# Kernel optimization log

Hardware: AMD Instinct MI355X
Metric: run time of the kernel (lower is better)

Reference implementation:

```python
import jax, jax.numpy as jnp
import numpy as np

N_GRAPHS = 64


def gcn_conv(x, W, b, src, dst, n_nodes):
    """PyG GCNConv: add self-loops, symmetric D^-1/2 (A+I) D^-1/2 normalization,
    linear transform, scatter-add aggregation at target nodes, plus bias."""
    xw = x @ W  # [N, out]  transform before propagate (PyG order)
    loop = jnp.arange(n_nodes, dtype=src.dtype)
    rows = jnp.concatenate([src, loop])  # message sources
    cols = jnp.concatenate([dst, loop])  # message targets
    deg = jax.ops.segment_sum(jnp.ones_like(cols, dtype=xw.dtype), cols,
                              num_segments=n_nodes)
    dinv = jnp.where(deg > 0, jax.lax.rsqrt(deg), 0.0)
    norm = dinv[rows] * dinv[cols]  # [E+N]
    msgs = norm[:, None] * xw[rows]  # gather + scale
    out = jax.ops.segment_sum(msgs, cols, num_segments=n_nodes)  # scatter-add
    return out + b


def global_mean_pool(x, batch, n_graphs):
    sums = jax.ops.segment_sum(x, batch, num_segments=n_graphs)
    cnts = jax.ops.segment_sum(jnp.ones((x.shape[0],), x.dtype), batch,
                               num_segments=n_graphs)
    return sums / jnp.maximum(cnts, 1.0)[:, None]


def setup_inputs() -> dict:
    key = jax.random.key(0)
    k1, k2, k3, k4, k5, k6 = jax.random.split(key, 6)
    N, E = 50000, 800000
    d_in, d_hid, d_out = 128, 128, 64
    x = jax.random.normal(k1, (N, d_in), dtype=jnp.float32)
    edge_index = jax.random.randint(k2, (2, E), 0, N, dtype=jnp.int64)
    batch = jnp.sort(jax.random.randint(k3, (N,), 0, N_GRAPHS, dtype=jnp.int64))
    # Glorot-ish init for GCN weights, zero bias (PyG default)
    W1 = jax.random.normal(k4, (d_in, d_hid), dtype=jnp.float32) / np.sqrt(d_in)
    b1 = jnp.zeros((d_hid,), jnp.float32)
    W2 = jax.random.normal(k5, (d_hid, d_out), dtype=jnp.float32) / np.sqrt(d_hid)
    b2 = jnp.zeros((d_out,), jnp.float32)
    return {"x": x, "edge_index": edge_index, "batch": batch,
            "W1": W1, "b1": b1, "W2": W2, "b2": b2}


def reference(x, edge_index, batch, W1, b1, W2, b2):
    n_nodes = x.shape[0]
    src, dst = edge_index[0], edge_index[1]
    h = jax.nn.relu(gcn_conv(x, W1, b1, src, dst, n_nodes))
    h = gcn_conv(h, W2, b2, src, dst, n_nodes)
    return global_mean_pool(h, batch, N_GRAPHS)
```

## Files before the change

### kernel.cpp

```cpp
#include <hip/hip_runtime.h>

typedef __attribute__((ext_vector_type(8))) short bf16x8;
typedef __attribute__((ext_vector_type(4))) float f32x4;

__device__ __forceinline__ unsigned short f2bf(float f) {
  unsigned u = __float_as_uint(f);
  u += 0x7FFFu + ((u >> 16) & 1u);
  return (unsigned short)(u >> 16);
}
__device__ __forceinline__ float bflo(unsigned u) { return __uint_as_float(u << 16); }
__device__ __forceinline__ float bfhi(unsigned u) { return __uint_as_float(u & 0xFFFF0000u); }

template <int CO, bool AF32>
__device__ __forceinline__ void gemm_body(const void* __restrict__ Aptr,
                                          const float* __restrict__ W,
                                          unsigned short* __restrict__ Y, int N,
                                          int bid, int tid, unsigned short* Wl) {
  constexpr int K = 128;
  constexpr int SP = K + 8;
  for (int i = tid; i < K * CO; i += 256) {
    int k = i / CO, n = i % CO;
    Wl[n * SP + k] = f2bf(W[i]);
  }
  __syncthreads();

  const int lane = tid & 63;
  const int quad = lane >> 4, l16 = lane & 15;
  const int mbase = bid * 64 + (tid >> 6) * 16;
  const int arow = min(mbase + l16, N - 1);

  bf16x8 afrag[4];
  if constexpr (AF32) {
    const float* A = (const float*)Aptr + (size_t)arow * K;
#pragma unroll
    for (int ks = 0; ks < 4; ks++) {
      const float4* p = (const float4*)(A + ks * 32 + quad * 8);
      float4 f0 = p[0], f1 = p[1];
      afrag[ks] = (bf16x8){(short)f2bf(f0.x), (short)f2bf(f0.y), (short)f2bf(f0.z), (short)f2bf(f0.w),
                           (short)f2bf(f1.x), (short)f2bf(f1.y), (short)f2bf(f1.z), (short)f2bf(f1.w)};
    }
  } else {
    const unsigned short* A = (const unsigned short*)Aptr + (size_t)arow * K;
#pragma unroll
    for (int ks = 0; ks < 4; ks++) afrag[ks] = *(const bf16x8*)(A + ks * 32 + quad * 8);
  }

#pragma unroll
  for (int ct = 0; ct < CO / 16; ct++) {
    f32x4 acc = {0.0f, 0.0f, 0.0f, 0.0f};
#pragma unroll
    for (int ks = 0; ks < 4; ks++) {
      bf16x8 b = *(const bf16x8*)(&Wl[(ct * 16 + l16) * SP + ks * 32 + quad * 8]);
      acc = __builtin_amdgcn_mfma_f32_16x16x32_bf16(afrag[ks], b, acc, 0, 0, 0);
    }
#pragma unroll
    for (int reg = 0; reg < 4; reg++) {
      int node = mbase + quad * 4 + reg;
      if (node < N) Y[(size_t)node * CO + ct * 16 + l16] = f2bf(acc[reg]);
    }
  }
}

__global__ __launch_bounds__(256) void k_mega1(const float* __restrict__ x,
                                               const float* __restrict__ W1,
                                               unsigned short* __restrict__ xw1b, int N,
                                               const int* __restrict__ dst,
                                               int* __restrict__ cnt,
                                               int* __restrict__ rank, int E,
                                               const int* __restrict__ batch,
                                               int* __restrict__ firstIdx,
                                               int gM, int gE4) {
  __shared__ unsigned short Wl[128 * 136];
  const int bid = blockIdx.x, tid = threadIdx.x;
  if (bid < gM) {
    gemm_body<128, true>(x, W1, xw1b, N, bid, tid, Wl);
  } else if (bid < gM + gE4) {
    int e0 = (bid - gM) * 1024 + tid * 4;
    if (e0 + 3 < E) {
      int4 d4 = *(const int4*)(dst + e0);
      int4 r;
      r.x = atomicAdd(&cnt[d4.x], 1);
      r.y = atomicAdd(&cnt[d4.y], 1);
      r.z = atomicAdd(&cnt[d4.z], 1);
      r.w = atomicAdd(&cnt[d4.w], 1);
      *(int4*)(rank + e0) = r;
    } else {
      for (int e = e0; e < E; e++) rank[e] = atomicAdd(&cnt[dst[e]], 1);
    }
  } else {
    int n = (bid - gM - gE4) * 256 + tid;
    if (n < N) {
      int b = batch[n];
      if (n == 0 || batch[n - 1] != b) firstIdx[b] = n + 1;
    }
  }
}

__global__ void k_seg(const int* __restrict__ cnt, int* __restrict__ start,
                      float* __restrict__ dinv, int* __restrict__ counter, int N) {
  const int v = blockIdx.x * 256 + threadIdx.x;
  const int lane = threadIdx.x & 63;
  int c = (v < N) ? cnt[v] : 0;
  int incl = c;
#pragma unroll
  for (int d = 1; d < 64; d <<= 1) {
    int t = __shfl_up(incl, d, 64);
    if (lane >= d) incl += t;
  }
  int base = 0;
  if (lane == 63) base = atomicAdd(counter, incl);
  base = __shfl(base, 63, 64);
  if (v < N) {
    start[v] = base + incl - c;
    dinv[v] = rsqrtf((float)(c + 1));
  }
}

__global__ void k_fill(const int* __restrict__ src, const int* __restrict__ dst,
                       const int* __restrict__ rank, const int* __restrict__ start,
                       const float* __restrict__ dinv, int2* __restrict__ colw, int E) {
  int e = blockIdx.x * 256 + threadIdx.x;
  if (e < E) {
    int s = src[e], d = dst[e];
    int p = start[d] + rank[e];
    float w = dinv[s] * dinv[d];
    colw[p] = make_int2(s, __float_as_int(w));
  }
}

__global__ __launch_bounds__(256) void k_agg128(const unsigned short* __restrict__ xwb,
                                                const float* __restrict__ dinv,
                                                const int* __restrict__ start,
                                                const int* __restrict__ cnt,
                                                const int2* __restrict__ colw,
                                                const float* __restrict__ bias,
                                                unsigned short* __restrict__ out, int N) {
  __shared__ int2 sEdge[4][64];
  const int tid = threadIdx.x;
  const int lane = tid & 63;
  const int wv = tid >> 6;
  const int slot = lane >> 4;
  const int fl = lane & 15;
  const int v = blockIdx.x * 4 + wv;
  if (v >= N) return;

  float acc[8] = {0.f, 0.f, 0.f, 0.f, 0.f, 0.f, 0.f, 0.f};
  const float dv = dinv[v];
  const float d2 = dv * dv;
  if (slot == 0) {
    uint4 s = *(const uint4*)((const char*)xwb + (((size_t)v << 8) | (fl << 4)));
    acc[0] += d2 * bflo(s.x); acc[1] += d2 * bfhi(s.x);
    acc[2] += d2 * bflo(s.y); acc[3] += d2 * bfhi(s.y);
    acc[4] += d2 * bflo(s.z); acc[5] += d2 * bfhi(s.z);
    acc[6] += d2 * bflo(s.w); acc[7] += d2 * bfhi(s.w);
  }

  const int j0 = start[v], jc = cnt[v];
  for (int base = 0; base < jc; base += 64) {
    int2 cw = (base + lane < jc) ? colw[j0 + base + lane] : make_int2(0, 0);
    sEdge[wv][lane] = cw;
    int m = jc - base;
    if (m > 64) m = 64;
    const int rounds = (m + 3) >> 2;
    const int rp = (rounds + 3) & ~3;
    for (int t = 0; t < rp; t += 4) {
      uint4 rbuf[4];
      float wbuf[4];
#pragma unroll
      for (int r = 0; r < 4; r++) {
        int2 e = sEdge[wv][(t + r) * 4 + slot];
        wbuf[r] = __int_as_float(e.y);
        rbuf[r] = *(const uint4*)((const char*)xwb + (((unsigned)e.x << 8) | (fl << 4)));
      }
#pragma unroll
      for (int r = 0; r < 4; r++) {
        const float w = wbuf[r];
        const uint4 rr = rbuf[r];
        acc[0] += w * bflo(rr.x); acc[1] += w * bfhi(rr.x);
        acc[2] += w * bflo(rr.y); acc[3] += w * bfhi(rr.y);
        acc[4] += w * bflo(rr.z); acc[5] += w * bfhi(rr.z);
        acc[6] += w * bflo(rr.w); acc[7] += w * bfhi(rr.w);
      }
    }
  }

#pragma unroll
  for (int d = 16; d < 64; d <<= 1)
#pragma unroll
    for (int k = 0; k < 8; k++) acc[k] += __shfl_xor(acc[k], d, 64);

  if (slot == 0) {
    float4 b0 = ((const float4*)bias)[fl * 2];
    float4 b1 = ((const float4*)bias)[fl * 2 + 1];
    float a0 = fmaxf(acc[0] + b0.x, 0.f), a1 = fmaxf(acc[1] + b0.y, 0.f);
    float a2 = fmaxf(acc[2] + b0.z, 0.f), a3 = fmaxf(acc[3] + b0.w, 0.f);
    float a4 = fmaxf(acc[4] + b1.x, 0.f), a5 = fmaxf(acc[5] + b1.y, 0.f);
    float a6 = fmaxf(acc[6] + b1.z, 0.f), a7 = fmaxf(acc[7] + b1.w, 0.f);
    uint4 st;
    st.x = (unsigned)f2bf(a0) | ((unsigned)f2bf(a1) << 16);
    st.y = (unsigned)f2bf(a2) | ((unsigned)f2bf(a3) << 16);
    st.z = (unsigned)f2bf(a4) | ((unsigned)f2bf(a5) << 16);
    st.w = (unsigned)f2bf(a6) | ((unsigned)f2bf(a7) << 16);
    *(uint4*)((char*)out + (((size_t)v << 8) | (fl << 4))) = st;
  }
}

__global__ __launch_bounds__(256) void k_gemm2(const unsigned short* __restrict__ A,
                                               const float* __restrict__ W,
                                               unsigned short* __restrict__ Y, int N) {
  __shared__ unsigned short Wl[64 * 136];
  gemm_body<64, false>(A, W, Y, N, blockIdx.x, threadIdx.x, Wl);
}

__global__ __launch_bounds__(256) void k_aggpool(const unsigned short* __restrict__ xwb,
                                                 const float* __restrict__ dinv,
                                                 const int* __restrict__ start,
                                                 const int* __restrict__ cnt,
                                                 const int2* __restrict__ colw,
                                                 const int* __restrict__ batch,
                                                 float* __restrict__ stage, int N) {
  __shared__ int2 sEdge[4][64];
  __shared__ float sAcc[4][64];
  const int tid = threadIdx.x;
  const int lane = tid & 63;
  const int wv = tid >> 6;
  const int slot = lane >> 3;
  const int fl = lane & 7;
  const int v = blockIdx.x * 4 + wv;

  float acc[8] = {0.f, 0.f, 0.f, 0.f, 0.f, 0.f, 0.f, 0.f};
  int b = 0;
  if (v < N) {
    b = batch[v];
    const float dv = dinv[v];
    const float d2 = dv * dv;
    if (slot == 0) {
      uint4 s = *(const uint4*)((const char*)xwb + (((size_t)v << 7) | (fl << 4)));
      acc[0] += d2 * bflo(s.x); acc[1] += d2 * bfhi(s.x);
      acc[2] += d2 * bflo(s.y); acc[3] += d2 * bfhi(s.y);
      acc[4] += d2 * bflo(s.z); acc[5] += d2 * bfhi(s.z);
      acc[6] += d2 * bflo(s.w); acc[7] += d2 * bfhi(s.w);
    }
    const int j0 = start[v], jc = cnt[v];
    for (int base = 0; base < jc; base += 64) {
      int2 cw = (base + lane < jc) ? colw[j0 + base + lane] : make_int2(0, 0);
      sEdge[wv][lane] = cw;
      int m = jc - base;
      if (m > 64) m = 64;
      const int rounds = (m + 7) >> 3;
      const int rp = (rounds + 3) & ~3;
      for (int t = 0; t < rp; t += 4) {
        uint4 rbuf[4];
        float wbuf[4];
#pragma unroll
        for (int r = 0; r < 4; r++) {
          int2 e = sEdge[wv][(t + r) * 8 + slot];
          wbuf[r] = __int_as_float(e.y);
          rbuf[r] = *(const uint4*)((const char*)xwb + (((unsigned)e.x << 7) | (fl << 4)));
        }
#pragma unroll
        for (int r = 0; r < 4; r++) {
          const float w = wbuf[r];
          const uint4 rr = rbuf[r];
          acc[0] += w * bflo(rr.x); acc[1] += w * bfhi(rr.x);
          acc[2] += w * bflo(rr.y); acc[3] += w * bfhi(rr.y);
          acc[4] += w * bflo(rr.z); acc[5] += w * bfhi(rr.z);
          acc[6] += w * bflo(rr.w); acc[7] += w * bfhi(rr.w);
        }
      }
    }
#pragma unroll
    for (int d = 8; d < 64; d <<= 1)
#pragma unroll
      for (int k = 0; k < 8; k++) acc[k] += __shfl_xor(acc[k], d, 64);
  }

  if (slot == 0) {
    *(float4*)&sAcc[wv][fl * 8] = make_float4(acc[0], acc[1], acc[2], acc[3]);
    *(float4*)&sAcc[wv][fl * 8 + 4] = make_float4(acc[4], acc[5], acc[6], acc[7]);
  }
  __syncthreads();

  const int v0 = blockIdx.x * 4;
  const int b0 = batch[min(v0, N - 1)];
  const int b3 = batch[min(v0 + 3, N - 1)];
  if ((b0 == b3) && (v0 + 3 < N)) {
    if (wv == 0) {
      float t = sAcc[0][lane] + sAcc[1][lane] + sAcc[2][lane] + sAcc[3][lane];
      atomicAdd(&stage[b0 * 64 + lane], t);
    }
  } else if (v < N) {
    atomicAdd(&stage[b * 64 + lane], sAcc[wv][lane]);
  }
}

__global__ void k_final(const float* __restrict__ stage, const int* __restrict__ firstIdx,
                        const float* __restrict__ b2, float* __restrict__ out, int N) {
  __shared__ float denom[64];
  const int tid = threadIdx.x;
  if (tid < 64) {
    int raw = firstIdx[tid];
    int fi = (raw > 0) ? raw - 1 : 0x7FFFFFFF;
    int m = fi;
#pragma unroll
    for (int d = 1; d < 64; d <<= 1) {
      int t = __shfl_down(m, d, 64);
      if (tid + d < 64) m = min(m, t);
    }
    int nxtm = __shfl_down(m, 1, 64);
    int nxt = (tid == 63) ? N : min(nxtm, N);
    int c = (fi == 0x7FFFFFFF) ? 0 : (nxt - fi);
    denom[tid] = fmaxf((float)c, 1.0f);
  }
  __syncthreads();
  for (int i = tid; i < 64 * 64; i += 256)
    out[i] = stage[i] / denom[i >> 6] + b2[i & 63];
}


extern "C" void kernel_launch(void* const* d_in, const int* in_sizes, int n_in,
                              void* d_out, int out_size, void* d_ws, size_t ws_size,
                              hipStream_t stream) {
  const float* x     = (const float*)d_in[0];
  const int*   ei    = (const int*)d_in[1];
  const int*   batch = (const int*)d_in[2];
  const float* W1    = (const float*)d_in[3];
  const float* b1    = (const float*)d_in[4];
  const float* W2    = (const float*)d_in[5];
  const float* b2    = (const float*)d_in[6];

  const int N = in_sizes[2];
  const int E = in_sizes[1] / 2;
  const int* src  = ei;
  const int* dstv = ei + E;

  unsigned short* xw1b = (unsigned short*)d_ws;
  unsigned short* h1b  = xw1b + (size_t)N * 128;
  unsigned short* xw2b = xw1b;
  int*   cnt     = (int*)(h1b + (size_t)N * 128);
  int*   counter = cnt + N;
  int*   firstIdx= counter + 1;
  float* stage   = (float*)(firstIdx + 64);
  int*   startv  = (int*)(stage + 4096);
  float* dinv    = (float*)(startv + N);
  int2*  colw    = (int2*)(((uintptr_t)(dinv + N) + 15) & ~(uintptr_t)15);
  int*   rank    = (int*)(colw + E);
  float* outp    = (float*)d_out;

  hipMemsetAsync(cnt, 0, (size_t)(N + 1 + 64 + 4096) * sizeof(int), stream);

  const int gM  = (N + 63) / 64;
  const int gE4 = (E + 1023) / 1024;
  const int gE  = (E + 255) / 256;
  const int gN  = (N + 255) / 256;
  const int gA  = (N + 3) / 4;

  k_mega1<<<gM + gE4 + gN, 256, 0, stream>>>(x, W1, xw1b, N, dstv, cnt, rank, E,
                                             batch, firstIdx, gM, gE4);
  k_seg<<<gN, 256, 0, stream>>>(cnt, startv, dinv, counter, N);
  k_fill<<<gE, 256, 0, stream>>>(src, dstv, rank, startv, dinv, colw, E);

  k_agg128<<<gA, 256, 0, stream>>>(xw1b, dinv, startv, cnt, colw, b1, h1b, N);

  k_gemm2<<<gM, 256, 0, stream>>>(h1b, W2, xw2b, N);
  k_aggpool<<<gA, 256, 0, stream>>>(xw2b, dinv, startv, cnt, colw, batch, stage, N);

  k_final<<<1, 256, 0, stream>>>(stage, firstIdx, b2, outp, N);
}
```

Before: 233.0 us.

## Map one node per lane-group in aggregation kernels, broadcast edges via shuffles

Both aggregation kernels now assign one destination node to each 16-lane (or 8-lane) group instead of one node per wavefront, so a wave processes 4 or 8 nodes at once. Edge metadata is loaded per group and broadcast with shuffles instead of being staged in shared memory, and the cross-group reduction is gone. This targets the lane waste that comes from low-degree nodes (about 16 edges on average) being spread across a full wave. The cost is divergence, since each wave iterates up to the largest degree in its group, and non-uniform pool blocks now issue per-element atomics.

```diff
diff --git a/kernel.cpp b/kernel.cpp
--- a/kernel.cpp
+++ b/kernel.cpp
@@ -135,42 +135,44 @@
                                                 const int2* __restrict__ colw,
                                                 const float* __restrict__ bias,
                                                 unsigned short* __restrict__ out, int N) {
-  __shared__ int2 sEdge[4][64];
   const int tid = threadIdx.x;
   const int lane = tid & 63;
+  const int gl = lane & 15;
+  const int grp = lane >> 4;
   const int wv = tid >> 6;
-  const int slot = lane >> 4;
-  const int fl = lane & 15;
-  const int v = blockIdx.x * 4 + wv;
-  if (v >= N) return;
-
-  float acc[8] = {0.f, 0.f, 0.f, 0.f, 0.f, 0.f, 0.f, 0.f};
-  const float dv = dinv[v];
-  const float d2 = dv * dv;
-  if (slot == 0) {
-    uint4 s = *(const uint4*)((const char*)xwb + (((size_t)v << 8) | (fl << 4)));
-    acc[0] += d2 * bflo(s.x); acc[1] += d2 * bfhi(s.x);
-    acc[2] += d2 * bflo(s.y); acc[3] += d2 * bfhi(s.y);
-    acc[4] += d2 * bflo(s.z); acc[5] += d2 * bfhi(s.z);
-    acc[6] += d2 * bflo(s.w); acc[7] += d2 * bfhi(s.w);
-  }
-
-  const int j0 = start[v], jc = cnt[v];
-  for (int base = 0; base < jc; base += 64) {
-    int2 cw = (base + lane < jc) ? colw[j0 + base + lane] : make_int2(0, 0);
-    sEdge[wv][lane] = cw;
-    int m = jc - base;
-    if (m > 64) m = 64;
-    const int rounds = (m + 3) >> 2;
-    const int rp = (rounds + 3) & ~3;
+  const int v = blockIdx.x * 16 + wv * 4 + grp;
+  const int vc = min(v, N - 1);
+
+  const float dv = dinv[vc];
+  const int j0 = start[vc];
+  const int jc = (v < N) ? cnt[vc] : 0;
+
+  float acc[8];
+  {
+    const float d2 = dv * dv;
+    uint4 s = *(const uint4*)((const char*)xwb + (((size_t)vc << 8) | (gl << 4)));
+    acc[0] = d2 * bflo(s.x); acc[1] = d2 * bfhi(s.x);
+    acc[2] = d2 * bflo(s.y); acc[3] = d2 * bfhi(s.y);
+    acc[4] = d2 * bflo(s.z); acc[5] = d2 * bfhi(s.z);
+    acc[6] = d2 * bflo(s.w); acc[7] = d2 * bfhi(s.w);
+  }
+
+  const int gbase = grp << 4;
+  for (int base = 0; __any(base < jc); base += 16) {
+    int2 cw = (base + gl < jc) ? colw[j0 + base + gl] : make_int2(0, 0);
+    int mv = jc - base;
+    mv = mv < 0 ? 0 : (mv > 16 ? 16 : mv);
+    int mm = max(mv, __shfl_xor(mv, 16, 64));
+    mm = max(mm, __shfl_xor(mm, 32, 64));
+    const int rp = (mm + 3) & ~3;
     for (int t = 0; t < rp; t += 4) {
       uint4 rbuf[4];
       float wbuf[4];
 #pragma unroll
       for (int r = 0; r < 4; r++) {
-        int2 e = sEdge[wv][(t + r) * 4 + slot];
-        wbuf[r] = __int_as_float(e.y);
-        rbuf[r] = *(const uint4*)((const char*)xwb + (((unsigned)e.x << 8) | (fl << 4)));
+        int sx = __shfl(cw.x, gbase + t + r, 64);
+        wbuf[r] = __int_as_float(__shfl(cw.y, gbase + t + r, 64));
+        rbuf[r] = *(const uint4*)((const char*)xwb + (((unsigned)sx << 8) | (gl << 4)));
       }
 #pragma unroll
       for (int r = 0; r < 4; r++) {
@@ -184,14 +186,9 @@
     }
   }
 
-#pragma unroll
-  for (int d = 16; d < 64; d <<= 1)
-#pragma unroll
-    for (int k = 0; k < 8; k++) acc[k] += __shfl_xor(acc[k], d, 64);
-
-  if (slot == 0) {
-    float4 b0 = ((const float4*)bias)[fl * 2];
-    float4 b1 = ((const float4*)bias)[fl * 2 + 1];
+  if (v < N) {
+    float4 b0 = ((const float4*)bias)[gl * 2];
+    float4 b1 = ((const float4*)bias)[gl * 2 + 1];
     float a0 = fmaxf(acc[0] + b0.x, 0.f), a1 = fmaxf(acc[1] + b0.y, 0.f);
     float a2 = fmaxf(acc[2] + b0.z, 0.f), a3 = fmaxf(acc[3] + b0.w, 0.f);
     float a4 = fmaxf(acc[4] + b1.x, 0.f), a5 = fmaxf(acc[5] + b1.y, 0.f);
@@ -201,7 +198,7 @@
     st.y = (unsigned)f2bf(a2) | ((unsigned)f2bf(a3) << 16);
     st.z = (unsigned)f2bf(a4) | ((unsigned)f2bf(a5) << 16);
     st.w = (unsigned)f2bf(a6) | ((unsigned)f2bf(a7) << 16);
-    *(uint4*)((char*)out + (((size_t)v << 8) | (fl << 4))) = st;
+    *(uint4*)((char*)out + (((size_t)v << 8) | (gl << 4))) = st;
   }
 }
 
@@ -219,78 +216,79 @@
                                                  const int2* __restrict__ colw,
                                                  const int* __restrict__ batch,
                                                  float* __restrict__ stage, int N) {
-  __shared__ int2 sEdge[4][64];
   __shared__ float sAcc[4][64];
   const int tid = threadIdx.x;
   const int lane = tid & 63;
+  const int gl = lane & 7;
+  const int grp = lane >> 3;
   const int wv = tid >> 6;
-  const int slot = lane >> 3;
-  const int fl = lane & 7;
-  const int v = blockIdx.x * 4 + wv;
-
-  float acc[8] = {0.f, 0.f, 0.f, 0.f, 0.f, 0.f, 0.f, 0.f};
-  int b = 0;
-  if (v < N) {
-    b = batch[v];
-    const float dv = dinv[v];
-    const float d2 = dv * dv;
-    if (slot == 0) {
-      uint4 s = *(const uint4*)((const char*)xwb + (((size_t)v << 7) | (fl << 4)));
-      acc[0] += d2 * bflo(s.x); acc[1] += d2 * bfhi(s.x);
-      acc[2] += d2 * bflo(s.y); acc[3] += d2 * bfhi(s.y);
-      acc[4] += d2 * bflo(s.z); acc[5] += d2 * bfhi(s.z);
-      acc[6] += d2 * bflo(s.w); acc[7] += d2 * bfhi(s.w);
-    }
-    const int j0 = start[v], jc = cnt[v];
-    for (int base = 0; base < jc; base += 64) {
-      int2 cw = (base + lane < jc) ? colw[j0 + base + lane] : make_int2(0, 0);
-      sEdge[wv][lane] = cw;
-      int m = jc - base;
-      if (m > 64) m = 64;
-      const int rounds = (m + 7) >> 3;
-      const int rp = (rounds + 3) & ~3;
-      for (int t = 0; t < rp; t += 4) {
-        uint4 rbuf[4];
-        float wbuf[4];
-#pragma unroll
-        for (int r = 0; r < 4; r++) {
-          int2 e = sEdge[wv][(t + r) * 8 + slot];
-          wbuf[r] = __int_as_float(e.y);
-          rbuf[r] = *(const uint4*)((const char*)xwb + (((unsigned)e.x << 7) | (fl << 4)));
-        }
-#pragma unroll
-        for (int r = 0; r < 4; r++) {
-          const float w = wbuf[r];
-          const uint4 rr = rbuf[r];
-          acc[0] += w * bflo(rr.x); acc[1] += w * bfhi(rr.x);
-          acc[2] += w * bflo(rr.y); acc[3] += w * bfhi(rr.y);
-          acc[4] += w * bflo(rr.z); acc[5] += w * bfhi(rr.z);
-          acc[6] += w * bflo(rr.w); acc[7] += w * bfhi(rr.w);
-        }
+  const int v = blockIdx.x * 32 + wv * 8 + grp;
+  const int vc = min(v, N - 1);
+
+  const float dv = dinv[vc];
+  const int j0 = start[vc];
+  const int jc = (v < N) ? cnt[vc] : 0;
+  const int b = batch[vc];
+
+  float acc[8];
+  {
+    const float d2 = (v < N) ? dv * dv : 0.0f;
+    uint4 s = *(const uint4*)((const char*)xwb + (((size_t)vc << 7) | (gl << 4)));
+    acc[0] = d2 * bflo(s.x); acc[1] = d2 * bfhi(s.x);
+    acc[2] = d2 * bflo(s.y); acc[3] = d2 * bfhi(s.y);
+    acc[4] = d2 * bflo(s.z); acc[5] = d2 * bfhi(s.z);
+    acc[6] = d2 * bflo(s.w); acc[7] = d2 * bfhi(s.w);
+  }
+
+  const int gbase = grp << 3;
+  for (int base = 0; __any(base < jc); base += 8) {
+    int2 cw = (base + gl < jc) ? colw[j0 + base + gl] : make_int2(0, 0);
+    int mv = jc - base;
+    mv = mv < 0 ? 0 : (mv > 8 ? 8 : mv);
+    int mm = max(mv, __shfl_xor(mv, 8, 64));
+    mm = max(mm, __shfl_xor(mm, 16, 64));
+    mm = max(mm, __shfl_xor(mm, 32, 64));
+    const int rp = (mm + 3) & ~3;
+    for (int t = 0; t < rp; t += 4) {
+      uint4 rbuf[4];
+      float wbuf[4];
+#pragma unroll
+      for (int r = 0; r < 4; r++) {
+        int sx = __shfl(cw.x, gbase + t + r, 64);
+        wbuf[r] = __int_as_float(__shfl(cw.y, gbase + t + r, 64));
+        rbuf[r] = *(const uint4*)((const char*)xwb + (((unsigned)sx << 7) | (gl << 4)));
       }
-    }
+#pragma unroll
+      for (int r = 0; r < 4; r++) {
+        const float w = wbuf[r];
+        const uint4 rr = rbuf[r];
+        acc[0] += w * bflo(rr.x); acc[1] += w * bfhi(rr.x);
+        acc[2] += w * bflo(rr.y); acc[3] += w * bfhi(rr.y);
+        acc[4] += w * bflo(rr.z); acc[5] += w * bfhi(rr.z);
+        acc[6] += w * bflo(rr.w); acc[7] += w * bfhi(rr.w);
+      }
+    }
+  }
+
+  const int v0 = blockIdx.x * 32;
+  const bool uniform = (v0 + 31 < N) && (batch[v0] == batch[v0 + 31]);
+  if (uniform) {
 #pragma unroll
     for (int d = 8; d < 64; d <<= 1)
 #pragma unroll
       for (int k = 0; k < 8; k++) acc[k] += __shfl_xor(acc[k], d, 64);
-  }
-
-  if (slot == 0) {
-    *(float4*)&sAcc[wv][fl * 8] = make_float4(acc[0], acc[1], acc[2], acc[3]);
-    *(float4*)&sAcc[wv][fl * 8 + 4] = make_float4(acc[4], acc[5], acc[6], acc[7]);
-  }
-  __syncthreads();
-
-  const int v0 = blockIdx.x * 4;
-  const int b0 = batch[min(v0, N - 1)];
-  const int b3 = batch[min(v0 + 3, N - 1)];
-  if ((b0 == b3) && (v0 + 3 < N)) {
+    if (grp == 0) {
+      *(float4*)&sAcc[wv][gl * 8] = make_float4(acc[0], acc[1], acc[2], acc[3]);
+      *(float4*)&sAcc[wv][gl * 8 + 4] = make_float4(acc[4], acc[5], acc[6], acc[7]);
+    }
+    __syncthreads();
     if (wv == 0) {
       float t = sAcc[0][lane] + sAcc[1][lane] + sAcc[2][lane] + sAcc[3][lane];
-      atomicAdd(&stage[b0 * 64 + lane], t);
+      atomicAdd(&stage[batch[v0] * 64 + lane], t);
     }
   } else if (v < N) {
-    atomicAdd(&stage[b * 64 + lane], sAcc[wv][lane]);
+#pragma unroll
+    for (int k = 0; k < 8; k++) atomicAdd(&stage[b * 64 + gl * 8 + k], acc[k]);
   }
 }
 
@@ -353,17 +351,18 @@
   const int gE4 = (E + 1023) / 1024;
   const int gE  = (E + 255) / 256;
   const int gN  = (N + 255) / 256;
-  const int gA  = (N + 3) / 4;
+  const int gA1 = (N + 15) / 16;
+  const int gA2 = (N + 31) / 32;
 
   k_mega1<<<gM + gE4 + gN, 256, 0, stream>>>(x, W1, xw1b, N, dstv, cnt, rank, E,
                                              batch, firstIdx, gM, gE4);
   k_seg<<<gN, 256, 0, stream>>>(cnt, startv, dinv, counter, N);
   k_fill<<<gE, 256, 0, stream>>>(src, dstv, rank, startv, dinv, colw, E);
 
-  k_agg128<<<gA, 256, 0, stream>>>(xw1b, dinv, startv, cnt, colw, b1, h1b, N);
+  k_agg128<<<gA1, 256, 0, stream>>>(xw1b, dinv, startv, cnt, colw, b1, h1b, N);
 
   k_gemm2<<<gM, 256, 0, stream>>>(h1b, W2, xw2b, N);
-  k_aggpool<<<gA, 256, 0, stream>>>(xw2b, dinv, startv, cnt, colw, batch, stage, N);
+  k_aggpool<<<gA2, 256, 0, stream>>>(xw2b, dinv, startv, cnt, colw, batch, stage, N);
 
   k_final<<<1, 256, 0, stream>>>(stage, firstIdx, b2, outp, N);
 }
```

New measurement: 214.4 us. 1.09x faster.
